# Kernel tuning notes

Hardware: AMD Instinct MI355X
Metric: run time of the kernel (lower is better)

Reference implementation:

```python
import jax, jax.numpy as jnp
import numpy as np

IN_CH = 64
OUT_CH = 64
SEQ_LEN = 2048
MODES = 64  # modes2 = min(modes1, seq_len//2) = 64
SCALE = 1.0 / (IN_CH * OUT_CH)


def setup_inputs() -> dict:
    key = jax.random.key(0)
    k1, k2, k3 = jax.random.split(key, 3)
    x = jax.random.normal(k1, (32, 8, IN_CH, SEQ_LEN), dtype=jnp.float32)
    # torch.rand(...) complex init scaled by 1/(in*out): real & imag in [0, scale)
    wr = SCALE * jax.random.uniform(k2, (IN_CH, OUT_CH, MODES), dtype=jnp.float32)
    wi = SCALE * jax.random.uniform(k3, (IN_CH, OUT_CH, MODES), dtype=jnp.float32)
    return {"x": x, "wr": wr, "wi": wi}


def reference(x, wr, wi):
    # x: [B, H, E, N] real; weights complex [in, out, modes]
    N = x.shape[-1]
    w = jax.lax.complex(wr, wi)
    x_ft = jnp.fft.rfft(x)                       # [B, H, E, N//2+1] complex64
    a = x_ft[..., :MODES]                        # keep only low modes
    out_low = jnp.einsum('bjix,iox->bjox', a, w)  # per-mode complex matmul
    # zero-fill remaining frequency bins (equivalent to out_ft zeros + slice set)
    pad = N // 2 + 1 - MODES
    out_ft = jnp.pad(out_low, ((0, 0), (0, 0), (0, 0), (0, pad)))
    return jnp.fft.irfft(out_ft, n=N)            # [B, H, out_ch, N] real
```

## Files before the change

### kernel.cpp

```cpp
#include <hip/hip_runtime.h>
#include <hip/hip_bf16.h>


typedef __bf16 bf16x8 __attribute__((ext_vector_type(8)));
typedef float  f32x4  __attribute__((ext_vector_type(4)));

#define SEQ 2048
#define NM2 128
#define KS  4
#define TWO_PI_OVER_N 3.0679615757712823e-03f

__device__ __forceinline__ unsigned int rnbf(float f) {
  unsigned int u = __builtin_bit_cast(unsigned int, f);
  return (u + 0x7fffu + ((u >> 16) & 1u)) >> 16;
}
__device__ __forceinline__ unsigned int pack2(float a, float b) {
  return rnbf(a) | (rnbf(b) << 16);
}

typedef const __attribute__((address_space(1))) unsigned int gu32;
typedef __attribute__((address_space(3))) unsigned int lu32;

__global__ __launch_bounds__(256) void k_tables(unsigned short* __restrict__ t1sw,
                                                unsigned short* __restrict__ t2t) {
  int idx = blockIdx.x * 256 + threadIdx.x;
  int c = idx >> 11;
  int n = idx & 2047;
  int k = c & 63;
  float ph = (float)((k * n) & 2047) * TWO_PI_OVER_N;
  float s, co;
  sincosf(ph, &s, &co);
  float v1 = (c < 64) ? co : -s;
  float ck = (k == 0 ? 1.0f : 2.0f) * (1.0f / 2048.0f);
  float v2 = (c < 64) ? ck * co : -ck * s;
  int kt = n >> 6, part = (n >> 3) & 7, e = n & 7;
  unsigned off = (unsigned)kt * 16384u +
                 (((unsigned)(c * 128 + part * 16)) ^ (((unsigned)c & 7u) << 4)) + 2u * (unsigned)e;
  *(unsigned short*)((char*)t1sw + off) = (unsigned short)rnbf(v1);
  t2t[n * NM2 + c] = (unsigned short)rnbf(v2);
}

__global__ __launch_bounds__(256) void k_gemm1(const float* __restrict__ x,
                                               const unsigned short* __restrict__ t1sw,
                                               float* __restrict__ P) {
  __shared__ int4 lds4[(8192 + 16384) / 16];
  char* lds = (char*)lds4;
  const int tid = threadIdx.x;
  const int wave = tid >> 6, lane = tid & 63;
  const int mtile = blockIdx.x >> 2, ks = blockIdx.x & (KS - 1);
  const int r0 = mtile * 64;
  const int kbase = ks * (SEQ / KS);

  f32x4 acc[8] = {};

  const int row_s = tid >> 2;
  const int q_s = tid & 3;
  const float* xrow = x + (r0 + row_s) * SEQ + kbase + q_s * 16;
  const unsigned xorA = (unsigned)(row_s & 7) << 4;
  const unsigned sA0 = ((unsigned)(row_s * 128 + q_s * 32)) ^ xorA;
  const unsigned sA1 = ((unsigned)(row_s * 128 + q_s * 32 + 16)) ^ xorA;

  const char* t1base = (const char*)t1sw + (size_t)(kbase >> 6) * 16384;

  f32x4 f[4];
#pragma unroll
  for (int m = 0; m < 4; ++m) f[m] = *(const f32x4*)(xrow + m * 4);

  for (int it = 0; it < 8; ++it) {
    __syncthreads();
    unsigned pk[8];
#pragma unroll
    for (int m = 0; m < 4; ++m) {
      pk[2 * m]     = pack2(f[m][0], f[m][1]);
      pk[2 * m + 1] = pack2(f[m][2], f[m][3]);
    }
    uint4 w0; w0.x = pk[0]; w0.y = pk[1]; w0.z = pk[2]; w0.w = pk[3];
    uint4 w1; w1.x = pk[4]; w1.y = pk[5]; w1.z = pk[6]; w1.w = pk[7];
    *(uint4*)(lds + sA0) = w0;
    *(uint4*)(lds + sA1) = w1;
    const char* tg = t1base + it * 16384;
#pragma unroll
    for (int p = 0; p < 4; ++p) {
      __builtin_amdgcn_global_load_lds((gu32*)(tg + (p * 256 + tid) * 16),
                                       (lu32*)(lds + 8192 + (p * 256 + wave * 64) * 16),
                                       16, 0, 0);
    }
    if (it < 7) {
#pragma unroll
      for (int m = 0; m < 4; ++m) f[m] = *(const f32x4*)(xrow + (it + 1) * 64 + m * 4);
    }
    __syncthreads();
#pragma unroll
    for (int kss = 0; kss < 2; ++kss) {
      const int arow = wave * 16 + (lane & 15);
      const bf16x8 av = *(const bf16x8*)(lds +
          ((arow * 128 + kss * 64 + ((lane >> 4) * 16)) ^ ((unsigned)(arow & 7) << 4)));
#pragma unroll
      for (int t = 0; t < 8; ++t) {
        const int col = t * 16 + (lane & 15);
        const bf16x8 bv = *(const bf16x8*)(lds + 8192 +
            ((col * 128 + kss * 64 + ((lane >> 4) * 16)) ^ ((unsigned)(col & 7) << 4)));
        acc[t] = __builtin_amdgcn_mfma_f32_16x16x32_bf16(av, bv, acc[t], 0, 0, 0);
      }
    }
  }
  float* Pout = P + (size_t)ks * (16384 * NM2);
#pragma unroll
  for (int t = 0; t < 8; ++t) {
    const int col = t * 16 + (lane & 15);
#pragma unroll
    for (int j = 0; j < 4; ++j) {
      const int row = r0 + wave * 16 + (lane >> 4) * 4 + j;
      Pout[row * NM2 + col] = acc[t][j];
    }
  }
}

__global__ __launch_bounds__(256) void k_stage2(const float* __restrict__ P,
                                                const float* __restrict__ wr,
                                                const float* __restrict__ wi,
                                                unsigned short* __restrict__ Bx) {
  __shared__ float sA[4][64][64];
  const int b = blockIdx.x;
  const int bjc = b >> 2, oh = (b >> 1) & 1, kh = b & 1;
  const int k0 = kh * 32;
  const int tid = threadIdx.x;
#pragma unroll
  for (int p = 0; p < 16; ++p) {
    int fidx = tid + 256 * p;
    int row_lin = fidx >> 4, q = fidx & 15;
    int col = (q < 8) ? (k0 + q * 4) : (64 + k0 + (q - 8) * 4);
    const float* base = P + (size_t)(bjc * 256 + row_lin) * NM2 + col;
    f32x4 v0 = *(const f32x4*)(base);
    f32x4 v1 = *(const f32x4*)(base + 1 * 16384 * NM2);
    f32x4 v2 = *(const f32x4*)(base + 2 * 16384 * NM2);
    f32x4 v3 = *(const f32x4*)(base + 3 * 16384 * NM2);
    f32x4 v = (v0 + v1) + (v2 + v3);
    *(f32x4*)(&sA[row_lin >> 6][row_lin & 63][q * 4]) = v;
  }
  __syncthreads();
  const int o_l = tid >> 3, kg = tid & 7;
  const int o = oh * 32 + o_l;
  const int kb = k0 + kg * 4;
  f32x4 accr[4] = {};
  f32x4 acci[4] = {};
  for (int i = 0; i < 64; ++i) {
    f32x4 wrv = *(const f32x4*)(wr + (i * 64 + o) * 64 + kb);
    f32x4 wiv = *(const f32x4*)(wi + (i * 64 + o) * 64 + kb);
#pragma unroll
    for (int bj = 0; bj < 4; ++bj) {
      f32x4 ar = *(const f32x4*)(&sA[bj][i][kg * 4]);
      f32x4 ai = *(const f32x4*)(&sA[bj][i][32 + kg * 4]);
#pragma unroll
      for (int kk = 0; kk < 4; ++kk) {
        accr[bj][kk] += ar[kk] * wrv[kk] - ai[kk] * wiv[kk];
        acci[bj][kk] += ar[kk] * wiv[kk] + ai[kk] * wrv[kk];
      }
    }
  }
#pragma unroll
  for (int bj = 0; bj < 4; ++bj) {
    const int r = (bjc * 4 + bj) * 64 + o;
    uint2 vr; vr.x = pack2(accr[bj][0], accr[bj][1]); vr.y = pack2(accr[bj][2], accr[bj][3]);
    uint2 vi; vi.x = pack2(acci[bj][0], acci[bj][1]); vi.y = pack2(acci[bj][2], acci[bj][3]);
    *(uint2*)(Bx + r * NM2 + kb)      = vr;
    *(uint2*)(Bx + r * NM2 + 64 + kb) = vi;
  }
}

__global__ __launch_bounds__(256) void k_gemm2(const unsigned short* __restrict__ Bx,
                                               const unsigned short* __restrict__ t2t,
                                               float* __restrict__ out) {
  __shared__ int4 lds4[65536 / 16];
  char* lds = (char*)lds4;
  const int tid = threadIdx.x, wave = tid >> 6, lane = tid & 63;
  const int mb = blockIdx.x >> 4, nb = blockIdx.x & 15;
  const int r0 = mb * 128, n0 = nb * 128;
#pragma unroll
  for (int p = 0; p < 8; ++p) {
    int seg = tid + 256 * p;
    int row = seg >> 4, part = seg & 15;
    unsigned sw = (unsigned)((row * 256 + part * 16) ^ ((row & 7) << 4));
    int4 va = *(const int4*)(Bx + (r0 + row) * NM2 + part * 8);
    *(int4*)(lds + sw) = va;
    int4 vb = *(const int4*)(t2t + (n0 + row) * NM2 + part * 8);
    *(int4*)(lds + 32768 + sw) = vb;
  }
  __syncthreads();
  f32x4 acc[2][8] = {};
#pragma unroll
  for (int ks = 0; ks < 4; ++ks) {
    const int ar0 = wave * 32 + (lane & 15);
    const int ar1 = ar0 + 16;
    const int koff = ks * 64 + (lane >> 4) * 16;
    bf16x8 a0 = *(const bf16x8*)(lds + ((ar0 * 256 + koff) ^ ((unsigned)(ar0 & 7) << 4)));
    bf16x8 a1 = *(const bf16x8*)(lds + ((ar1 * 256 + koff) ^ ((unsigned)(ar1 & 7) << 4)));
#pragma unroll
    for (int t = 0; t < 8; ++t) {
      const int col = t * 16 + (lane & 15);
      bf16x8 bv = *(const bf16x8*)(lds + 32768 + ((col * 256 + koff) ^ ((unsigned)(col & 7) << 4)));
      acc[0][t] = __builtin_amdgcn_mfma_f32_16x16x32_bf16(a0, bv, acc[0][t], 0, 0, 0);
      acc[1][t] = __builtin_amdgcn_mfma_f32_16x16x32_bf16(a1, bv, acc[1][t], 0, 0, 0);
    }
  }
#pragma unroll
  for (int m = 0; m < 2; ++m) {
#pragma unroll
    for (int t = 0; t < 8; ++t) {
      const int col = n0 + t * 16 + (lane & 15);
#pragma unroll
      for (int j = 0; j < 4; ++j) {
        const int row = r0 + wave * 32 + m * 16 + (lane >> 4) * 4 + j;
        out[row * SEQ + col] = acc[m][t][j];
      }
    }
  }
}

extern "C" void kernel_launch(void* const* d_in, const int* in_sizes, int n_in,
                              void* d_out, int out_size, void* d_ws, size_t ws_size,
                              hipStream_t stream) {
  const float* x  = (const float*)d_in[0];
  const float* wr = (const float*)d_in[1];
  const float* wi = (const float*)d_in[2];
  float* out = (float*)d_out;
  char* ws = (char*)d_ws;
  unsigned short* t1sw = (unsigned short*)(ws);
  unsigned short* t2t  = (unsigned short*)(ws + 524288);
  float*          P    = (float*)(ws + 1048576);
  unsigned short* Bx   = (unsigned short*)(ws + 1048576 + (size_t)KS * 16384 * NM2 * 4);

  k_tables<<<dim3(1024), dim3(256), 0, stream>>>(t1sw, t2t);
  k_gemm1 <<<dim3(256 * KS), dim3(256), 0, stream>>>(x, t1sw, P);
  k_stage2<<<dim3(256),  dim3(256), 0, stream>>>(P, wr, wi, Bx);
  k_gemm2 <<<dim3(2048), dim3(256), 0, stream>>>(Bx, t2t, out);
}
```

Before: 105.4 us.

## Double-buffer gemm1 LDS tiles and store split-K partials as bf16

The forward DFT GEMM now double-buffers both the x tile and the twiddle tile in LDS. The next tile's async global-to-LDS load and x conversion overlap the current MFMAs, and the loop has one barrier per iteration instead of two. The split-K partial sums P are also written as bf16 instead of fp32, which halves the write and read traffic between gemm1 and stage2. The cost is more LDS per block (48KB), which may lower occupancy, and extra rounding error on the partial sums.

```diff
diff --git a/kernel.cpp b/kernel.cpp
--- a/kernel.cpp
+++ b/kernel.cpp
@@ -16,6 +16,9 @@
 }
 __device__ __forceinline__ unsigned int pack2(float a, float b) {
   return rnbf(a) | (rnbf(b) << 16);
+}
+__device__ __forceinline__ float frombf(unsigned int lo16_in_place) {
+  return __builtin_bit_cast(float, lo16_in_place);
 }
 
 typedef const __attribute__((address_space(1))) unsigned int gu32;
@@ -42,8 +45,8 @@
 
 __global__ __launch_bounds__(256) void k_gemm1(const float* __restrict__ x,
                                                const unsigned short* __restrict__ t1sw,
-                                               float* __restrict__ P) {
-  __shared__ int4 lds4[(8192 + 16384) / 16];
+                                               unsigned short* __restrict__ P) {
+  __shared__ int4 lds4[49152 / 16];
   char* lds = (char*)lds4;
   const int tid = threadIdx.x;
   const int wave = tid >> 6, lane = tid & 63;
@@ -55,7 +58,7 @@
 
   const int row_s = tid >> 2;
   const int q_s = tid & 3;
-  const float* xrow = x + (r0 + row_s) * SEQ + kbase + q_s * 16;
+  const float* xrow = x + (size_t)(r0 + row_s) * SEQ + kbase + q_s * 16;
   const unsigned xorA = (unsigned)(row_s & 7) << 4;
   const unsigned sA0 = ((unsigned)(row_s * 128 + q_s * 32)) ^ xorA;
   const unsigned sA1 = ((unsigned)(row_s * 128 + q_s * 32 + 16)) ^ xorA;
@@ -65,9 +68,13 @@
   f32x4 f[4];
 #pragma unroll
   for (int m = 0; m < 4; ++m) f[m] = *(const f32x4*)(xrow + m * 4);
-
-  for (int it = 0; it < 8; ++it) {
-    __syncthreads();
+#pragma unroll
+  for (int p = 0; p < 4; ++p) {
+    __builtin_amdgcn_global_load_lds((gu32*)(t1base + (p * 256 + tid) * 16),
+                                     (lu32*)(lds + 16384 + (p * 256 + wave * 64) * 16),
+                                     16, 0, 0);
+  }
+  {
     unsigned pk[8];
 #pragma unroll
     for (int m = 0; m < 4; ++m) {
@@ -78,45 +85,64 @@
     uint4 w1; w1.x = pk[4]; w1.y = pk[5]; w1.z = pk[6]; w1.w = pk[7];
     *(uint4*)(lds + sA0) = w0;
     *(uint4*)(lds + sA1) = w1;
-    const char* tg = t1base + it * 16384;
-#pragma unroll
-    for (int p = 0; p < 4; ++p) {
-      __builtin_amdgcn_global_load_lds((gu32*)(tg + (p * 256 + tid) * 16),
-                                       (lu32*)(lds + 8192 + (p * 256 + wave * 64) * 16),
-                                       16, 0, 0);
-    }
+  }
+  __syncthreads();
+
+  for (int it = 0; it < 8; ++it) {
+    const int cur = it & 1, nxt = cur ^ 1;
+    const int xoff = cur * 8192;
+    const int toff = 16384 + cur * 16384;
     if (it < 7) {
+      const char* tg = t1base + (it + 1) * 16384;
+#pragma unroll
+      for (int p = 0; p < 4; ++p) {
+        __builtin_amdgcn_global_load_lds((gu32*)(tg + (p * 256 + tid) * 16),
+                                         (lu32*)(lds + 16384 + nxt * 16384 + (p * 256 + wave * 64) * 16),
+                                         16, 0, 0);
+      }
 #pragma unroll
       for (int m = 0; m < 4; ++m) f[m] = *(const f32x4*)(xrow + (it + 1) * 64 + m * 4);
     }
-    __syncthreads();
 #pragma unroll
     for (int kss = 0; kss < 2; ++kss) {
       const int arow = wave * 16 + (lane & 15);
-      const bf16x8 av = *(const bf16x8*)(lds +
+      const bf16x8 av = *(const bf16x8*)(lds + xoff +
           ((arow * 128 + kss * 64 + ((lane >> 4) * 16)) ^ ((unsigned)(arow & 7) << 4)));
 #pragma unroll
       for (int t = 0; t < 8; ++t) {
         const int col = t * 16 + (lane & 15);
-        const bf16x8 bv = *(const bf16x8*)(lds + 8192 +
+        const bf16x8 bv = *(const bf16x8*)(lds + toff +
             ((col * 128 + kss * 64 + ((lane >> 4) * 16)) ^ ((unsigned)(col & 7) << 4)));
         acc[t] = __builtin_amdgcn_mfma_f32_16x16x32_bf16(av, bv, acc[t], 0, 0, 0);
       }
     }
-  }
-  float* Pout = P + (size_t)ks * (16384 * NM2);
+    if (it < 7) {
+      unsigned pk[8];
+#pragma unroll
+      for (int m = 0; m < 4; ++m) {
+        pk[2 * m]     = pack2(f[m][0], f[m][1]);
+        pk[2 * m + 1] = pack2(f[m][2], f[m][3]);
+      }
+      uint4 w0; w0.x = pk[0]; w0.y = pk[1]; w0.z = pk[2]; w0.w = pk[3];
+      uint4 w1; w1.x = pk[4]; w1.y = pk[5]; w1.z = pk[6]; w1.w = pk[7];
+      *(uint4*)(lds + nxt * 8192 + sA0) = w0;
+      *(uint4*)(lds + nxt * 8192 + sA1) = w1;
+    }
+    __syncthreads();
+  }
+  unsigned short* Pout = P + (size_t)ks * (16384 * NM2);
 #pragma unroll
   for (int t = 0; t < 8; ++t) {
     const int col = t * 16 + (lane & 15);
 #pragma unroll
     for (int j = 0; j < 4; ++j) {
       const int row = r0 + wave * 16 + (lane >> 4) * 4 + j;
-      Pout[row * NM2 + col] = acc[t][j];
-    }
-  }
-}
-
-__global__ __launch_bounds__(256) void k_stage2(const float* __restrict__ P,
+      Pout[row * NM2 + col] = (unsigned short)rnbf(acc[t][j]);
+    }
+  }
+}
+
+__global__ __launch_bounds__(256) void k_stage2(const unsigned short* __restrict__ P,
                                                 const float* __restrict__ wr,
                                                 const float* __restrict__ wi,
                                                 unsigned short* __restrict__ Bx) {
@@ -130,12 +156,16 @@
     int fidx = tid + 256 * p;
     int row_lin = fidx >> 4, q = fidx & 15;
     int col = (q < 8) ? (k0 + q * 4) : (64 + k0 + (q - 8) * 4);
-    const float* base = P + (size_t)(bjc * 256 + row_lin) * NM2 + col;
-    f32x4 v0 = *(const f32x4*)(base);
-    f32x4 v1 = *(const f32x4*)(base + 1 * 16384 * NM2);
-    f32x4 v2 = *(const f32x4*)(base + 2 * 16384 * NM2);
-    f32x4 v3 = *(const f32x4*)(base + 3 * 16384 * NM2);
-    f32x4 v = (v0 + v1) + (v2 + v3);
+    const unsigned short* base = P + (size_t)(bjc * 256 + row_lin) * NM2 + col;
+    f32x4 v = {};
+#pragma unroll
+    for (int s = 0; s < KS; ++s) {
+      uint2 u = *(const uint2*)(base + (size_t)s * (16384 * NM2));
+      v[0] += frombf(u.x << 16);
+      v[1] += frombf(u.x & 0xffff0000u);
+      v[2] += frombf(u.y << 16);
+      v[3] += frombf(u.y & 0xffff0000u);
+    }
     *(f32x4*)(&sA[row_lin >> 6][row_lin & 63][q * 4]) = v;
   }
   __syncthreads();
@@ -227,8 +257,8 @@
   char* ws = (char*)d_ws;
   unsigned short* t1sw = (unsigned short*)(ws);
   unsigned short* t2t  = (unsigned short*)(ws + 524288);
-  float*          P    = (float*)(ws + 1048576);
-  unsigned short* Bx   = (unsigned short*)(ws + 1048576 + (size_t)KS * 16384 * NM2 * 4);
+  unsigned short* P    = (unsigned short*)(ws + 1048576);
+  unsigned short* Bx   = (unsigned short*)(ws + 1048576 + (size_t)KS * 16384 * NM2 * 2);
 
   k_tables<<<dim3(1024), dim3(256), 0, stream>>>(t1sw, t2t);
   k_gemm1 <<<dim3(256 * KS), dim3(256), 0, stream>>>(x, t1sw, P);
```

After: 103.8 us. No clear change (-1.5%).
